# Kernel tuning notes

Measured on AMD Instinct MI355X. Metric: run time of the kernel, lower is better.

The kernel has to match this reference:

```python
import jax, jax.numpy as jnp
import numpy as np

N = 50000   # num_entities
F = 300     # node feature dim
D = 128     # embedding_dim
H = 4       # heads
C = D // H  # per-head out channels (32)
E = 640000  # num edges
R = 200     # num_relations
L = 2       # num_layers
NEG_SLOPE = 0.2  # PyG GATv2Conv default


def setup_inputs() -> dict:
    key = jax.random.key(0)
    ks = jax.random.split(key, 14)
    s = 0.1
    return {
        "entity": jnp.arange(N, dtype=jnp.int32),
        "edge_index": jax.random.randint(ks[0], (2, E), 0, N, dtype=jnp.int32),
        "edge_type": jax.random.randint(ks[1], (E,), 0, R, dtype=jnp.int32),
        # learned parameters
        "node_features": jax.random.normal(ks[2], (N, F), jnp.float32) * s,   # entity_embedding table
        "rel_emb": jax.random.normal(ks[3], (R, D), jnp.float32) * s,          # relation_embedding
        "proj_w": jax.random.normal(ks[4], (F, D), jnp.float32) * s,           # project Linear
        "proj_b": jnp.zeros((D,), jnp.float32),
        # per-layer GATv2Conv params, stacked over L layers
        "w_l": jax.random.normal(ks[5], (L, D, H * C), jnp.float32) * s,       # lin_l weight
        "b_l": jnp.zeros((L, H * C), jnp.float32),
        "w_r": jax.random.normal(ks[6], (L, D, H * C), jnp.float32) * s,       # lin_r weight
        "b_r": jnp.zeros((L, H * C), jnp.float32),
        "w_e": jax.random.normal(ks[7], (L, D, H * C), jnp.float32) * s,       # lin_edge weight (no bias)
        "att": jax.random.normal(ks[8], (L, H, C), jnp.float32) * s,           # attention vector a
        "bias": jnp.zeros((L, H * C), jnp.float32),                             # output bias
    }


def _gatv2_layer(x, src, dst, edge_attr, w_l, b_l, w_r, b_r, w_e, att, bias):
    # x: [N, D], edge_attr: [E, D]
    x_l = (x @ w_l + b_l).reshape(N, H, C)
    x_r = (x @ w_r + b_r).reshape(N, H, C)
    e = (edge_attr @ w_e).reshape(E, H, C)
    # per-edge message (gather src/dst + edge), GATv2: leaky_relu BEFORE attention dot
    m = jax.nn.leaky_relu(x_l[src] + x_r[dst] + e, NEG_SLOPE)   # [E, H, C]
    logits = jnp.einsum('ehc,hc->eh', m, att)                    # [E, H]
    # segment softmax over edges grouped by destination node
    lmax = jax.ops.segment_max(logits, dst, num_segments=N)      # [N, H]
    ex = jnp.exp(logits - lmax[dst])                             # [E, H]
    denom = jax.ops.segment_sum(ex, dst, num_segments=N)         # [N, H]
    alpha = ex / denom[dst]                                      # [E, H]
    # scatter-aggregate messages x_l[src] weighted by alpha
    out = jax.ops.segment_sum(x_l[src] * alpha[:, :, None], dst, num_segments=N)  # [N, H, C]
    return out.reshape(N, H * C) + bias


def reference(entity, edge_index, edge_type, node_features, rel_emb,
              proj_w, proj_b, w_l, b_l, w_r, b_r, w_e, att, bias):
    x = node_features[entity]            # embedding lookup
    x = x @ proj_w + proj_b              # project to D
    edge_attr = rel_emb[edge_type]       # [E, D] (weights=False -> no edge_weight scaling)
    src, dst = edge_index[0], edge_index[1]
    for i in range(L):
        x = _gatv2_layer(x, src, dst, edge_attr,
                         w_l[i], b_l[i], w_r[i], b_r[i], w_e[i], att[i], bias[i])
        if i != L - 1:
            x = jax.nn.elu(x)            # dropout inactive (eval mode)
    return x
```

## Files before the change

kernel.cpp:

```cpp
#include <hip/hip_runtime.h>

#define NN 50000
#define FF 300
#define DD 128
#define HH 4
#define CC 32
#define EE 640000
#define RR 200
#define LL 2
#define SB ((NN + 255) / 256)
#define PK 320
#define WTOT (128 * PK + 4 * 128 * 128)
#define HB ((EE + 255) / 256)
#define WB ((WTOT + 255) / 256)
#define RB (LL * RR / 2)

typedef unsigned short u16;
typedef unsigned int u32;
typedef __attribute__((ext_vector_type(8))) short short8;
typedef __attribute__((ext_vector_type(4))) float floatx4;

__device__ __forceinline__ float bf2f(u16 u) {
    union { u32 i; float f; } v; v.i = ((u32)u) << 16; return v.f;
}
__device__ __forceinline__ u16 f2bf(float f) {
    u32 u = __float_as_uint(f);
    u32 r = (u >> 16) & 1u;
    u += 0x7fffu + r;
    return (u16)(u >> 16);
}
__device__ __forceinline__ void bf2x(u32 p, float& lo, float& hi) {
    lo = __uint_as_float(p << 16);
    hi = __uint_as_float(p & 0xffff0000u);
}

__device__ __forceinline__ int block_excl_scan(int v, int* lds4, int* total) {
    int lane = threadIdx.x & 63, wid = threadIdx.x >> 6;
    int x = v;
    #pragma unroll
    for (int off = 1; off < 64; off <<= 1) {
        int y = __shfl_up(x, off, 64);
        if (lane >= off) x += y;
    }
    if (lane == 63) lds4[wid] = x;
    __syncthreads();
    int add = 0;
    #pragma unroll
    for (int w = 0; w < 4; w++) add += (w < wid) ? lds4[w] : 0;
    *total = lds4[0] + lds4[1] + lds4[2] + lds4[3];
    return x + add - v;
}

__global__ __launch_bounds__(256)
void prep_kernel(const int* __restrict__ ei, int* __restrict__ counts,
                 const float* __restrict__ proj_w, const float* __restrict__ w_l,
                 const float* __restrict__ w_r, u16* __restrict__ wt,
                 const float* __restrict__ rel_emb, const float* __restrict__ w_e,
                 float* __restrict__ erel)
{
    __shared__ float rv[2][DD];
    int b = blockIdx.x, tid = threadIdx.x;
    if (b < HB) {
        int e = b * 256 + tid;
        if (e < EE) atomicAdd(&counts[ei[EE + e]], 1);
    } else if (b < HB + WB) {
        int i = (b - HB) * 256 + tid;
        if (i < WTOT) {
            float v;
            if (i < 128 * PK) {
                int n = i / PK, k = i - n * PK;
                v = (k < FF) ? proj_w[(size_t)k * DD + n] : 0.f;
            } else {
                int j = i - 128 * PK;
                int seg = j >> 14;
                int r = j & 16383;
                int n = r >> 7, k = r & 127;
                const float* src = (seg < 2) ? (w_l + (size_t)seg * DD * DD)
                                             : (w_r + (size_t)(seg - 2) * DD * DD);
                v = src[(size_t)k * DD + n];
            }
            wt[i] = f2bf(v);
        }
    } else {
        int half = tid >> 7, d = tid & 127;
        int lr = (b - HB - WB) * 2 + half;
        int l = lr / RR, r = lr - l * RR;
        rv[half][d] = rel_emb[r * DD + d];
        __syncthreads();
        const float* W = w_e + (size_t)l * DD * DD;
        float acc = 0.f;
        #pragma unroll 8
        for (int k = 0; k < DD; k++) acc += rv[half][k] * W[k * DD + d];
        erel[(size_t)lr * DD + d] = acc;
    }
}

template<bool ABF16, bool GATHER>
__global__ __launch_bounds__(256)
void gemm_mfma_kernel(const void* __restrict__ A_, const int* __restrict__ rowidx,
                      int lda, int K, int Ka, int ldb,
                      const u16* __restrict__ BT1, const float* __restrict__ bias1,
                      u16* __restrict__ C1,
                      const u16* __restrict__ BT2, const float* __restrict__ bias2,
                      u16* __restrict__ C2, int M)
{
    const u16*   BT   = (blockIdx.y == 0) ? BT1 : BT2;
    const float* bias = (blockIdx.y == 0) ? bias1 : bias2;
    u16*         Cout = (blockIdx.y == 0) ? C1 : C2;

    __shared__ u16 As[128][72];
    __shared__ u16 Bs[128][72];
    int tid  = threadIdx.x;
    int m0   = blockIdx.x * 128;
    int wave = tid >> 6, lane = tid & 63;
    int quad = lane >> 4, l16 = lane & 15;
    int wrow = (wave >> 1) * 64, wcol = (wave & 1) * 64;

    floatx4 acc[4][4];
    #pragma unroll
    for (int i = 0; i < 4; i++)
        #pragma unroll
        for (int j = 0; j < 4; j++) acc[i][j] = (floatx4){0.f, 0.f, 0.f, 0.f};

    int ar = tid >> 1, ah = tid & 1;
    int arow = m0 + ar;
    int rid = (arow < M) ? (GATHER ? rowidx[arow] : arow) : 0;

    for (int kk = 0; kk < K; kk += 64) {
        #pragma unroll
        for (int q = 0; q < 2; q++) {
            int kb = kk + ah * 32 + q * 16;
            u16 tmp[16];
            if (ABF16) {
                const u16* Ap = (const u16*)A_ + (size_t)rid * lda + kb;
                if (kb + 16 <= Ka) {
                    *(short8*)&tmp[0] = *(const short8*)Ap;
                    *(short8*)&tmp[8] = *(const short8*)(Ap + 8);
                } else {
                    #pragma unroll
                    for (int j = 0; j < 16; j++) tmp[j] = (kb + j < Ka) ? Ap[j] : (u16)0;
                }
            } else {
                const float* Ap = (const float*)A_ + (size_t)rid * lda + kb;
                if (kb + 16 <= Ka) {
                    #pragma unroll
                    for (int qq = 0; qq < 4; qq++) {
                        float4 f = *(const float4*)(Ap + qq * 4);
                        tmp[qq*4+0] = f2bf(f.x); tmp[qq*4+1] = f2bf(f.y);
                        tmp[qq*4+2] = f2bf(f.z); tmp[qq*4+3] = f2bf(f.w);
                    }
                } else {
                    #pragma unroll
                    for (int j = 0; j < 16; j++) tmp[j] = (kb + j < Ka) ? f2bf(Ap[j]) : (u16)0;
                }
            }
            *(short8*)&As[ar][ah * 32 + q * 16]     = *(short8*)&tmp[0];
            *(short8*)&As[ar][ah * 32 + q * 16 + 8] = *(short8*)&tmp[8];
        }
        {
            const u16* Bp = BT + (size_t)ar * ldb + kk + ah * 32;
            #pragma unroll
            for (int q = 0; q < 4; q++)
                *(short8*)&Bs[ar][ah * 32 + q * 8] = *(const short8*)(Bp + q * 8);
        }
        __syncthreads();
        #pragma unroll
        for (int ks = 0; ks < 2; ks++) {
            short8 af[4], bfr[4];
            #pragma unroll
            for (int i = 0; i < 4; i++)
                af[i] = *(const short8*)&As[wrow + i * 16 + l16][ks * 32 + quad * 8];
            #pragma unroll
            for (int j = 0; j < 4; j++)
                bfr[j] = *(const short8*)&Bs[wcol + j * 16 + l16][ks * 32 + quad * 8];
            #pragma unroll
            for (int i = 0; i < 4; i++)
                #pragma unroll
                for (int j = 0; j < 4; j++)
                    acc[i][j] = __builtin_amdgcn_mfma_f32_16x16x32_bf16(
                        af[i], bfr[j], acc[i][j], 0, 0, 0);
        }
        __syncthreads();
    }

    #pragma unroll
    for (int i = 0; i < 4; i++) {
        #pragma unroll
        for (int rr = 0; rr < 4; rr++) {
            int row = m0 + wrow + i * 16 + quad * 4 + rr;
            if (row < M) {
                #pragma unroll
                for (int j = 0; j < 4; j++) {
                    int col = wcol + j * 16 + l16;
                    Cout[(size_t)row * DD + col] = f2bf(acc[i][j][rr] + bias[col]);
                }
            }
        }
    }
}

__global__ __launch_bounds__(256)
void scan_local_kernel(const int* __restrict__ counts, int* __restrict__ offsets,
                       int* __restrict__ bsum)
{
    __shared__ int lds4[4];
    int i = blockIdx.x * 256 + threadIdx.x;
    int v = (i < NN) ? counts[i] : 0;
    int total;
    int ex = block_excl_scan(v, lds4, &total);
    if (i < NN) offsets[i] = ex;
    if (threadIdx.x == 0) bsum[blockIdx.x] = total;
}

__global__ __launch_bounds__(256)
void scan_bsum_kernel(int* __restrict__ bsum)
{
    __shared__ int lds4[4];
    int t = threadIdx.x;
    int v = (t < SB) ? bsum[t] : 0;
    int total;
    int ex = block_excl_scan(v, lds4, &total);
    if (t < SB) bsum[t] = ex;
}

__global__ __launch_bounds__(256)
void scatter_kernel(const int* __restrict__ ei, const int* __restrict__ et,
                    const int* __restrict__ offsets, const int* __restrict__ bsum,
                    int* __restrict__ fill, u32* __restrict__ dstorder)
{
    int e = blockIdx.x * 256 + threadIdx.x;
    if (e >= EE) return;
    int d = ei[EE + e];
    int pos = offsets[d] + bsum[d >> 8] + atomicAdd(&fill[d], 1);
    dstorder[pos] = (u32)ei[e] | ((u32)et[e] << 16);
}

__global__ __launch_bounds__(256)
void node_kernel(const u32* __restrict__ dstorder, const int* __restrict__ offsets,
                 const int* __restrict__ bsum,
                 const u16* __restrict__ xl, const u16* __restrict__ xr,
                 const float* __restrict__ erel, const float* __restrict__ att,
                 const float* __restrict__ bias,
                 u16* __restrict__ xnext, float* __restrict__ outp, int is_last)
{
    int tid  = threadIdx.x;
    int node = blockIdx.x * 4 + (tid >> 6);
    int lane = tid & 63;
    if (node >= NN) return;
    int g  = lane >> 4;
    int gl = lane & 15;
    int c0 = gl * 8;
    int beg = offsets[node] + bsum[node >> 8];
    int end = (node == NN - 1) ? EE : offsets[node + 1] + bsum[(node + 1) >> 8];

    float xrf[8], attf[8];
    {
        const u32* xp = (const u32*)&xr[(size_t)node * DD + c0];
        #pragma unroll
        for (int q = 0; q < 4; q++) bf2x(xp[q], xrf[q*2], xrf[q*2+1]);
        float4 a0 = *(const float4*)&att[c0];
        float4 a1 = *(const float4*)&att[c0 + 4];
        attf[0]=a0.x; attf[1]=a0.y; attf[2]=a0.z; attf[3]=a0.w;
        attf[4]=a1.x; attf[5]=a1.y; attf[6]=a1.z; attf[7]=a1.w;
    }

    float s = 0.f;
    float a[8];
    #pragma unroll
    for (int j = 0; j < 8; j++) a[j] = 0.f;

    for (int base = beg; base < end; base += 4) {
        int es = base + g;
        bool valid = es < end;
        u32 st = valid ? dstorder[es] : 0;
        int src = st & 0xffff;
        int typ = st >> 16;
        const u32*   xp = (const u32*)&xl[(size_t)src * DD + c0];
        const float* ep = erel + (size_t)typ * DD + c0;
        u32 xv0 = xp[0], xv1 = xp[1], xv2 = xp[2], xv3 = xp[3];
        float4 e0 = *(const float4*)ep;
        float4 e1 = *(const float4*)(ep + 4);
        float xf[8];
        bf2x(xv0, xf[0], xf[1]); bf2x(xv1, xf[2], xf[3]);
        bf2x(xv2, xf[4], xf[5]); bf2x(xv3, xf[6], xf[7]);
        float ef[8] = {e0.x, e0.y, e0.z, e0.w, e1.x, e1.y, e1.z, e1.w};
        float p = 0.f;
        #pragma unroll
        for (int j = 0; j < 8; j++) {
            float m = xf[j] + xrf[j] + ef[j];
            m = fmaxf(m, 0.2f * m);
            p += m * attf[j];
        }
        p += __shfl_xor(p, 1, 64);
        p += __shfl_xor(p, 2, 64);
        float w = valid ? __expf(fminf(p, 60.f)) : 0.f;
        s += w;
        #pragma unroll
        for (int j = 0; j < 8; j++) a[j] += w * xf[j];
    }

    #pragma unroll
    for (int j = 0; j < 8; j++) {
        a[j] += __shfl_xor(a[j], 16, 64);
        a[j] += __shfl_xor(a[j], 32, 64);
    }
    s += __shfl_xor(s, 16, 64);
    s += __shfl_xor(s, 32, 64);

    if (lane < 16) {
        float rh = 1.f / fmaxf(s, 1e-30f);
        float4 b0 = *(const float4*)&bias[c0];
        float4 b1 = *(const float4*)&bias[c0 + 4];
        float bv[8] = {b0.x, b0.y, b0.z, b0.w, b1.x, b1.y, b1.z, b1.w};
        float v[8];
        #pragma unroll
        for (int j = 0; j < 8; j++) v[j] = a[j] * rh + bv[j];
        if (is_last) {
            float4* op = (float4*)&outp[(size_t)node * DD + c0];
            op[0] = make_float4(v[0], v[1], v[2], v[3]);
            op[1] = make_float4(v[4], v[5], v[6], v[7]);
        } else {
            u16 pk[8];
            #pragma unroll
            for (int j = 0; j < 8; j++) {
                float w2 = v[j] > 0.f ? v[j] : __expf(v[j]) - 1.f;
                pk[j] = f2bf(w2);
            }
            *(short8*)&xnext[(size_t)node * DD + c0] = *(short8*)pk;
        }
    }
}

extern "C" void kernel_launch(void* const* d_in, const int* in_sizes, int n_in,
                              void* d_out, int out_size, void* d_ws, size_t ws_size,
                              hipStream_t stream)
{
    const int*   entity        = (const int*)d_in[0];
    const int*   edge_index    = (const int*)d_in[1];
    const int*   edge_type     = (const int*)d_in[2];
    const float* node_features = (const float*)d_in[3];
    const float* rel_emb       = (const float*)d_in[4];
    const float* proj_w        = (const float*)d_in[5];
    const float* proj_b        = (const float*)d_in[6];
    const float* w_l           = (const float*)d_in[7];
    const float* b_l           = (const float*)d_in[8];
    const float* w_r           = (const float*)d_in[9];
    const float* b_r           = (const float*)d_in[10];
    const float* w_e           = (const float*)d_in[11];
    const float* att           = (const float*)d_in[12];
    const float* bias          = (const float*)d_in[13];

    u16*   xb      = (u16*)d_ws;
    u16*   xl      = xb + (size_t)NN * DD;
    u16*   xr      = xl + (size_t)NN * DD;
    float* erel    = (float*)(xr + (size_t)NN * DD);
    u16*   wt      = (u16*)(erel + (size_t)LL * RR * DD);
    u32*   dstorder= (u32*)(wt + WTOT);
    int*   counts  = (int*)(dstorder + (size_t)EE);
    int*   fill    = counts + NN;
    int*   offsets = fill + NN;
    int*   bsum    = offsets + NN;

    hipMemsetAsync(counts, 0, (size_t)NN * 2 * sizeof(int), stream);
    prep_kernel<<<HB + WB + RB, 256, 0, stream>>>(
        edge_index, counts, proj_w, w_l, w_r, wt, rel_emb, w_e, erel);

    scan_local_kernel<<<SB, 256, 0, stream>>>(counts, offsets, bsum);
    scan_bsum_kernel<<<1, 256, 0, stream>>>(bsum);
    scatter_kernel<<<(EE + 255) / 256, 256, 0, stream>>>(
        edge_index, edge_type, offsets, bsum, fill, dstorder);

    const u16* wtProj = wt;
    const int GB = (NN + 127) / 128;
    gemm_mfma_kernel<false, true><<<dim3(GB, 1), 256, 0, stream>>>(
        node_features, entity, FF, PK, FF, PK,
        wtProj, proj_b, xb, wtProj, proj_b, xb, NN);

    for (int l = 0; l < LL; l++) {
        const u16* wtl = wt + 128 * PK + l * 16384;
        const u16* wtr = wt + 128 * PK + 32768 + l * 16384;
        gemm_mfma_kernel<true, false><<<dim3(GB, 2), 256, 0, stream>>>(
            xb, nullptr, DD, DD, DD, DD,
            wtl, b_l + l * DD, xl,
            wtr, b_r + l * DD, xr, NN);

        node_kernel<<<(NN + 3) / 4, 256, 0, stream>>>(
            dstorder, offsets, bsum, xl, xr, erel + (size_t)l * RR * DD,
            att + (size_t)l * DD, bias + (size_t)l * DD,
            xb, (float*)d_out, l == LL - 1);
    }
}
```

Baseline: 340.9 us.

## Switch intermediates from bf16 to fp16 and use packed half math in edge loop

Converts all stored intermediates (weights, x_l/x_r, relation-edge projections) from bf16 to fp16, and the GEMMs from bf16 MFMA to fp16 MFMA. The per-edge attention loop now uses packed half2 adds, max and dot2 instructions, and accumulates the weighted messages in half2 instead of fp32. The erel table shrinks to half width, which reduces gather bandwidth. In exchange, accumulating many edge contributions in fp16 risks precision loss or overflow for unnormalized exp weights up to e^60.

```diff
diff --git a/kernel.cpp b/kernel.cpp
--- a/kernel.cpp
+++ b/kernel.cpp
@@ -17,21 +17,32 @@
 
 typedef unsigned short u16;
 typedef unsigned int u32;
-typedef __attribute__((ext_vector_type(8))) short short8;
+typedef _Float16 h2   __attribute__((ext_vector_type(2)));
+typedef _Float16 half8 __attribute__((ext_vector_type(8)));
 typedef __attribute__((ext_vector_type(4))) float floatx4;
 
-__device__ __forceinline__ float bf2f(u16 u) {
-    union { u32 i; float f; } v; v.i = ((u32)u) << 16; return v.f;
-}
-__device__ __forceinline__ u16 f2bf(float f) {
-    u32 u = __float_as_uint(f);
-    u32 r = (u >> 16) & 1u;
-    u += 0x7fffu + r;
-    return (u16)(u >> 16);
-}
-__device__ __forceinline__ void bf2x(u32 p, float& lo, float& hi) {
-    lo = __uint_as_float(p << 16);
-    hi = __uint_as_float(p & 0xffff0000u);
+__device__ __forceinline__ u16 f2h(float f) {
+    union { _Float16 h; u16 u; } v; v.h = (_Float16)f; return v.u;
+}
+__device__ __forceinline__ float h2f(u16 u) {
+    union { u16 u; _Float16 h; } v; v.u = u; return (float)v.h;
+}
+__device__ __forceinline__ h2 u2h2(u32 p) {
+    union { u32 u; h2 h; } v; v.u = p; return v.h;
+}
+__device__ __forceinline__ h2 hmax2(h2 a, h2 b) {
+#if __has_builtin(__builtin_elementwise_max)
+    return __builtin_elementwise_max(a, b);
+#else
+    h2 r; r.x = a.x > b.x ? a.x : b.x; r.y = a.y > b.y ? a.y : b.y; return r;
+#endif
+}
+__device__ __forceinline__ float hdot2(h2 a, h2 b, float c) {
+#if __has_builtin(__builtin_amdgcn_fdot2)
+    return __builtin_amdgcn_fdot2(a, b, c, false);
+#else
+    return c + (float)a.x * (float)b.x + (float)a.y * (float)b.y;
+#endif
 }
 
 __device__ __forceinline__ int block_excl_scan(int v, int* lds4, int* total) {
@@ -56,7 +67,7 @@
                  const float* __restrict__ proj_w, const float* __restrict__ w_l,
                  const float* __restrict__ w_r, u16* __restrict__ wt,
                  const float* __restrict__ rel_emb, const float* __restrict__ w_e,
-                 float* __restrict__ erel)
+                 u16* __restrict__ erel)
 {
     __shared__ float rv[2][DD];
     int b = blockIdx.x, tid = threadIdx.x;
@@ -79,7 +90,7 @@
                                              : (w_r + (size_t)(seg - 2) * DD * DD);
                 v = src[(size_t)k * DD + n];
             }
-            wt[i] = f2bf(v);
+            wt[i] = f2h(v);
         }
     } else {
         int half = tid >> 7, d = tid & 127;
@@ -91,11 +102,11 @@
         float acc = 0.f;
         #pragma unroll 8
         for (int k = 0; k < DD; k++) acc += rv[half][k] * W[k * DD + d];
-        erel[(size_t)lr * DD + d] = acc;
-    }
-}
-
-template<bool ABF16, bool GATHER>
+        erel[(size_t)lr * DD + d] = f2h(acc);
+    }
+}
+
+template<bool AF16, bool GATHER>
 __global__ __launch_bounds__(256)
 void gemm_mfma_kernel(const void* __restrict__ A_, const int* __restrict__ rowidx,
                       int lda, int K, int Ka, int ldb,
@@ -131,11 +142,11 @@
         for (int q = 0; q < 2; q++) {
             int kb = kk + ah * 32 + q * 16;
             u16 tmp[16];
-            if (ABF16) {
+            if (AF16) {
                 const u16* Ap = (const u16*)A_ + (size_t)rid * lda + kb;
                 if (kb + 16 <= Ka) {
-                    *(short8*)&tmp[0] = *(const short8*)Ap;
-                    *(short8*)&tmp[8] = *(const short8*)(Ap + 8);
+                    *(half8*)&tmp[0] = *(const half8*)Ap;
+                    *(half8*)&tmp[8] = *(const half8*)(Ap + 8);
                 } else {
                     #pragma unroll
                     for (int j = 0; j < 16; j++) tmp[j] = (kb + j < Ka) ? Ap[j] : (u16)0;
@@ -146,38 +157,38 @@
                     #pragma unroll
                     for (int qq = 0; qq < 4; qq++) {
                         float4 f = *(const float4*)(Ap + qq * 4);
-                        tmp[qq*4+0] = f2bf(f.x); tmp[qq*4+1] = f2bf(f.y);
-                        tmp[qq*4+2] = f2bf(f.z); tmp[qq*4+3] = f2bf(f.w);
+                        tmp[qq*4+0] = f2h(f.x); tmp[qq*4+1] = f2h(f.y);
+                        tmp[qq*4+2] = f2h(f.z); tmp[qq*4+3] = f2h(f.w);
                     }
                 } else {
                     #pragma unroll
-                    for (int j = 0; j < 16; j++) tmp[j] = (kb + j < Ka) ? f2bf(Ap[j]) : (u16)0;
+                    for (int j = 0; j < 16; j++) tmp[j] = (kb + j < Ka) ? f2h(Ap[j]) : (u16)0;
                 }
             }
-            *(short8*)&As[ar][ah * 32 + q * 16]     = *(short8*)&tmp[0];
-            *(short8*)&As[ar][ah * 32 + q * 16 + 8] = *(short8*)&tmp[8];
+            *(half8*)&As[ar][ah * 32 + q * 16]     = *(half8*)&tmp[0];
+            *(half8*)&As[ar][ah * 32 + q * 16 + 8] = *(half8*)&tmp[8];
         }
         {
             const u16* Bp = BT + (size_t)ar * ldb + kk + ah * 32;
             #pragma unroll
             for (int q = 0; q < 4; q++)
-                *(short8*)&Bs[ar][ah * 32 + q * 8] = *(const short8*)(Bp + q * 8);
+                *(half8*)&Bs[ar][ah * 32 + q * 8] = *(const half8*)(Bp + q * 8);
         }
         __syncthreads();
         #pragma unroll
         for (int ks = 0; ks < 2; ks++) {
-            short8 af[4], bfr[4];
+            half8 af[4], bfr[4];
             #pragma unroll
             for (int i = 0; i < 4; i++)
-                af[i] = *(const short8*)&As[wrow + i * 16 + l16][ks * 32 + quad * 8];
+                af[i] = *(const half8*)&As[wrow + i * 16 + l16][ks * 32 + quad * 8];
             #pragma unroll
             for (int j = 0; j < 4; j++)
-                bfr[j] = *(const short8*)&Bs[wcol + j * 16 + l16][ks * 32 + quad * 8];
+                bfr[j] = *(const half8*)&Bs[wcol + j * 16 + l16][ks * 32 + quad * 8];
             #pragma unroll
             for (int i = 0; i < 4; i++)
                 #pragma unroll
                 for (int j = 0; j < 4; j++)
-                    acc[i][j] = __builtin_amdgcn_mfma_f32_16x16x32_bf16(
+                    acc[i][j] = __builtin_amdgcn_mfma_f32_16x16x32_f16(
                         af[i], bfr[j], acc[i][j], 0, 0, 0);
         }
         __syncthreads();
@@ -192,7 +203,7 @@
                 #pragma unroll
                 for (int j = 0; j < 4; j++) {
                     int col = wcol + j * 16 + l16;
-                    Cout[(size_t)row * DD + col] = f2bf(acc[i][j][rr] + bias[col]);
+                    Cout[(size_t)row * DD + col] = f2h(acc[i][j][rr] + bias[col]);
                 }
             }
         }
@@ -239,7 +250,7 @@
 void node_kernel(const u32* __restrict__ dstorder, const int* __restrict__ offsets,
                  const int* __restrict__ bsum,
                  const u16* __restrict__ xl, const u16* __restrict__ xr,
-                 const float* __restrict__ erel, const float* __restrict__ att,
+                 const u16* __restrict__ erel, const float* __restrict__ att,
                  const float* __restrict__ bias,
                  u16* __restrict__ xnext, float* __restrict__ outp, int is_last)
 {
@@ -253,21 +264,23 @@
     int beg = offsets[node] + bsum[node >> 8];
     int end = (node == NN - 1) ? EE : offsets[node + 1] + bsum[(node + 1) >> 8];
 
-    float xrf[8], attf[8];
+    h2 xrh[4], atth[4];
     {
         const u32* xp = (const u32*)&xr[(size_t)node * DD + c0];
         #pragma unroll
-        for (int q = 0; q < 4; q++) bf2x(xp[q], xrf[q*2], xrf[q*2+1]);
-        float4 a0 = *(const float4*)&att[c0];
-        float4 a1 = *(const float4*)&att[c0 + 4];
-        attf[0]=a0.x; attf[1]=a0.y; attf[2]=a0.z; attf[3]=a0.w;
-        attf[4]=a1.x; attf[5]=a1.y; attf[6]=a1.z; attf[7]=a1.w;
-    }
+        for (int q = 0; q < 4; q++) xrh[q] = u2h2(xp[q]);
+        #pragma unroll
+        for (int q = 0; q < 4; q++) {
+            float2 av = *(const float2*)&att[c0 + q * 2];
+            atth[q] = (h2){(_Float16)av.x, (_Float16)av.y};
+        }
+    }
+    const h2 c02 = (h2){(_Float16)0.2f, (_Float16)0.2f};
 
     float s = 0.f;
-    float a[8];
-    #pragma unroll
-    for (int j = 0; j < 8; j++) a[j] = 0.f;
+    h2 a2[4];
+    #pragma unroll
+    for (int q = 0; q < 4; q++) a2[q] = (h2){(_Float16)0.f, (_Float16)0.f};
 
     for (int base = beg; base < end; base += 4) {
         int es = base + g;
@@ -275,30 +288,29 @@
         u32 st = valid ? dstorder[es] : 0;
         int src = st & 0xffff;
         int typ = st >> 16;
-        const u32*   xp = (const u32*)&xl[(size_t)src * DD + c0];
-        const float* ep = erel + (size_t)typ * DD + c0;
-        u32 xv0 = xp[0], xv1 = xp[1], xv2 = xp[2], xv3 = xp[3];
-        float4 e0 = *(const float4*)ep;
-        float4 e1 = *(const float4*)(ep + 4);
-        float xf[8];
-        bf2x(xv0, xf[0], xf[1]); bf2x(xv1, xf[2], xf[3]);
-        bf2x(xv2, xf[4], xf[5]); bf2x(xv3, xf[6], xf[7]);
-        float ef[8] = {e0.x, e0.y, e0.z, e0.w, e1.x, e1.y, e1.z, e1.w};
+        const u32* xp = (const u32*)&xl[(size_t)src * DD + c0];
+        const u32* ep = (const u32*)&erel[(size_t)typ * DD + c0];
+        h2 xh[4];
         float p = 0.f;
         #pragma unroll
-        for (int j = 0; j < 8; j++) {
-            float m = xf[j] + xrf[j] + ef[j];
-            m = fmaxf(m, 0.2f * m);
-            p += m * attf[j];
+        for (int q = 0; q < 4; q++) {
+            xh[q] = u2h2(xp[q]);
+            h2 m = (xh[q] + xrh[q]) + u2h2(ep[q]);
+            m = hmax2(m, m * c02);
+            p = hdot2(m, atth[q], p);
         }
         p += __shfl_xor(p, 1, 64);
         p += __shfl_xor(p, 2, 64);
         float w = valid ? __expf(fminf(p, 60.f)) : 0.f;
         s += w;
-        #pragma unroll
-        for (int j = 0; j < 8; j++) a[j] += w * xf[j];
-    }
-
+        h2 wh = (h2){(_Float16)w, (_Float16)w};
+        #pragma unroll
+        for (int q = 0; q < 4; q++) a2[q] += wh * xh[q];
+    }
+
+    float a[8];
+    #pragma unroll
+    for (int q = 0; q < 4; q++) { a[q*2] = (float)a2[q].x; a[q*2+1] = (float)a2[q].y; }
     #pragma unroll
     for (int j = 0; j < 8; j++) {
         a[j] += __shfl_xor(a[j], 16, 64);
@@ -324,9 +336,9 @@
             #pragma unroll
             for (int j = 0; j < 8; j++) {
                 float w2 = v[j] > 0.f ? v[j] : __expf(v[j]) - 1.f;
-                pk[j] = f2bf(w2);
+                pk[j] = f2h(w2);
             }
-            *(short8*)&xnext[(size_t)node * DD + c0] = *(short8*)pk;
+            *(half8*)&xnext[(size_t)node * DD + c0] = *(half8*)pk;
         }
     }
 }
@@ -353,8 +365,8 @@
     u16*   xb      = (u16*)d_ws;
     u16*   xl      = xb + (size_t)NN * DD;
     u16*   xr      = xl + (size_t)NN * DD;
-    float* erel    = (float*)(xr + (size_t)NN * DD);
-    u16*   wt      = (u16*)(erel + (size_t)LL * RR * DD);
+    u16*   erel    = xr + (size_t)NN * DD;
+    u16*   wt      = erel + (size_t)LL * RR * DD;
     u32*   dstorder= (u32*)(wt + WTOT);
     int*   counts  = (int*)(dstorder + (size_t)EE);
     int*   fill    = counts + NN;
```

Result: no change. 334.8 us (-1.8%).
